# Kernel tuning notes

Hardware: AMD Instinct MI355X
Metric: run time of the kernel (lower is better)

## Reference

```python
import jax, jax.numpy as jnp
import numpy as np


def setup_inputs() -> dict:
    key = jax.random.key(0)
    kf, kz = jax.random.split(key)
    B, H, S = 32, 1024, 2048
    f = jax.random.uniform(kf, (B, H, S), dtype=jnp.float32)  # forget gate in [0,1]
    z = jax.random.normal(kz, (B, H, S), dtype=jnp.float32)
    return {"f": f, "z": z}


def reference(f, z):
    # Original: permute (B,H,S)->(S,B,H), run h_t = (1-f_t)*z_t + f_t*h_{t-1}
    # with h_{-1}=0, then permute back (S,B,H)->(B,H,S).
    fs = jnp.moveaxis(f, 2, 0)  # (S,B,H)
    zs = jnp.moveaxis(z, 2, 0)  # (S,B,H)
    h0 = jnp.zeros(f.shape[:2], dtype=f.dtype)  # (B,H)

    def step(h_prev, fz):
        ft, zt = fz
        h = (1.0 - ft) * zt + ft * h_prev
        return h, h

    _, hs = jax.lax.scan(step, h0, (fs, zs))  # hs: (S,B,H)
    return jnp.moveaxis(hs, 0, 2)  # (B,H,S)
```

## Files before the change

kernel.cpp:

```cpp
#include <hip/hip_runtime.h>


#define SEQ_LEN 2048
#define THREADS 256
#define PER_THREAD 8

__global__ __launch_bounds__(THREADS) void fpool_scan_kernel(
    const float* __restrict__ f,
    const float* __restrict__ z,
    float* __restrict__ out)
{
    const long long row  = blockIdx.x;
    const long long base = row * (long long)SEQ_LEN;
    const int tid  = threadIdx.x;
    const int lane = tid & 63;
    const int wave = tid >> 6;

    const float4* f4 = reinterpret_cast<const float4*>(f + base);
    const float4* z4 = reinterpret_cast<const float4*>(z + base);
    float4 fa = f4[tid * 2 + 0];
    float4 fb = f4[tid * 2 + 1];
    float4 za = z4[tid * 2 + 0];
    float4 zb = z4[tid * 2 + 1];

    float av[PER_THREAD] = {fa.x, fa.y, fa.z, fa.w, fb.x, fb.y, fb.z, fb.w};
    float zv[PER_THREAD] = {za.x, za.y, za.z, za.w, zb.x, zb.y, zb.z, zb.w};

    float P[PER_THREAD], L[PER_THREAD];
    float p = 1.0f, l = 0.0f;
#pragma unroll
    for (int i = 0; i < PER_THREAD; ++i) {
        const float ai = av[i];
        const float bi = (1.0f - ai) * zv[i];
        l = fmaf(ai, l, bi);
        p = p * ai;
        P[i] = p;
        L[i] = l;
    }

    float cp = p, cl = l;
#pragma unroll
    for (int d = 1; d < 64; d <<= 1) {
        float pp = __shfl_up(cp, d);
        float pl = __shfl_up(cl, d);
        if (lane >= d) {
            cl = fmaf(cp, pl, cl);
            cp = cp * pp;
        }
    }

    __shared__ float wp[THREADS / 64];
    __shared__ float wl[THREADS / 64];
    if (lane == 63) { wp[wave] = cp; wl[wave] = cl; }
    __syncthreads();

    float h_wave = 0.0f;
#pragma unroll
    for (int w = 0; w < THREADS / 64; ++w) {
        if (w < wave) h_wave = fmaf(wp[w], h_wave, wl[w]);
    }

    float ep = __shfl_up(cp, 1);
    float el = __shfl_up(cl, 1);
    if (lane == 0) { ep = 1.0f; el = 0.0f; }

    const float h_in = fmaf(ep, h_wave, el);

    float o[PER_THREAD];
#pragma unroll
    for (int i = 0; i < PER_THREAD; ++i) o[i] = fmaf(P[i], h_in, L[i]);

    float4* o4 = reinterpret_cast<float4*>(out + base);
    o4[tid * 2 + 0] = make_float4(o[0], o[1], o[2], o[3]);
    o4[tid * 2 + 1] = make_float4(o[4], o[5], o[6], o[7]);
}

extern "C" void kernel_launch(void* const* d_in, const int* in_sizes, int n_in,
                              void* d_out, int out_size, void* d_ws, size_t ws_size,
                              hipStream_t stream) {
    const float* f = reinterpret_cast<const float*>(d_in[0]);
    const float* z = reinterpret_cast<const float*>(d_in[1]);
    float* out = reinterpret_cast<float*>(d_out);

    const long long total = in_sizes[0];
    const int rows = (int)(total / SEQ_LEN);

    fpool_scan_kernel<<<rows, THREADS, 0, stream>>>(f, z, out);
}
```

Baseline: 142.5 us.

## Split each row into two coalesced halves with separate block scans and nontemporal stores

Each thread now loads one float4 from each half of the row, so every load instruction is fully contiguous across the block instead of strided by two float4s per thread. Each half gets its own wave-shuffle and cross-wave scan, and the second half is seeded with the total of the first. Outputs go out through nontemporal stores to avoid polluting cache. In exchange the shuffle scan work and block barriers are doubled, which adds latency to a kernel that is mostly bound by memory bandwidth.

```diff
diff --git a/kernel.cpp b/kernel.cpp
--- a/kernel.cpp
+++ b/kernel.cpp
@@ -3,7 +3,44 @@
 
 #define SEQ_LEN 2048
 #define THREADS 256
-#define PER_THREAD 8
+#define CHUNK   4
+
+typedef float fvec4 __attribute__((ext_vector_type(4)));
+
+__device__ __forceinline__ void scan_block(
+    float p, float l, int lane, int wave,
+    float* wp, float* wl,
+    float& ep, float& el, float& tp, float& tl)
+{
+    float cp = p, cl = l;
+#pragma unroll
+    for (int d = 1; d < 64; d <<= 1) {
+        float pp = __shfl_up(cp, d);
+        float pl = __shfl_up(cl, d);
+        if (lane >= d) {
+            cl = fmaf(cp, pl, cl);
+            cp = cp * pp;
+        }
+    }
+    if (lane == 63) { wp[wave] = cp; wl[wave] = cl; }
+    __syncthreads();
+
+    ep = __shfl_up(cp, 1);
+    el = __shfl_up(cl, 1);
+    if (lane == 0) { ep = 1.0f; el = 0.0f; }
+
+    float bp = 1.0f, bl = 0.0f;
+    float qp = 1.0f, ql = 0.0f;
+#pragma unroll
+    for (int w = 0; w < THREADS / 64; ++w) {
+        float wpw = wp[w], wlw = wl[w];
+        if (w < wave) { bl = fmaf(wpw, bl, wlw); bp *= wpw; }
+        ql = fmaf(wpw, ql, wlw); qp *= wpw;
+    }
+    el = fmaf(ep, bl, el);
+    ep = ep * bp;
+    tp = qp; tl = ql;
+}
 
 __global__ __launch_bounds__(THREADS) void fpool_scan_kernel(
     const float* __restrict__ f,
@@ -18,61 +55,64 @@
 
     const float4* f4 = reinterpret_cast<const float4*>(f + base);
     const float4* z4 = reinterpret_cast<const float4*>(z + base);
-    float4 fa = f4[tid * 2 + 0];
-    float4 fb = f4[tid * 2 + 1];
-    float4 za = z4[tid * 2 + 0];
-    float4 zb = z4[tid * 2 + 1];
+    fvec4* o4 = reinterpret_cast<fvec4*>(out + base);
 
-    float av[PER_THREAD] = {fa.x, fa.y, fa.z, fa.w, fb.x, fb.y, fb.z, fb.w};
-    float zv[PER_THREAD] = {za.x, za.y, za.z, za.w, zb.x, zb.y, zb.z, zb.w};
+    float4 fA = f4[tid];
+    float4 zA = z4[tid];
+    float4 fB = f4[THREADS + tid];
+    float4 zB = z4[THREADS + tid];
 
-    float P[PER_THREAD], L[PER_THREAD];
-    float p = 1.0f, l = 0.0f;
+    float aA[CHUNK] = {fA.x, fA.y, fA.z, fA.w};
+    float vA[CHUNK] = {zA.x, zA.y, zA.z, zA.w};
+    float aB[CHUNK] = {fB.x, fB.y, fB.z, fB.w};
+    float vB[CHUNK] = {zB.x, zB.y, zB.z, zB.w};
+
+    float PA[CHUNK], LA[CHUNK], PB[CHUNK], LB[CHUNK];
+    {
+        float p = 1.0f, l = 0.0f;
 #pragma unroll
-    for (int i = 0; i < PER_THREAD; ++i) {
-        const float ai = av[i];
-        const float bi = (1.0f - ai) * zv[i];
-        l = fmaf(ai, l, bi);
-        p = p * ai;
-        P[i] = p;
-        L[i] = l;
+        for (int i = 0; i < CHUNK; ++i) {
+            l = fmaf(aA[i], l, (1.0f - aA[i]) * vA[i]);
+            p = p * aA[i];
+            PA[i] = p; LA[i] = l;
+        }
     }
-
-    float cp = p, cl = l;
+    {
+        float p = 1.0f, l = 0.0f;
 #pragma unroll
-    for (int d = 1; d < 64; d <<= 1) {
-        float pp = __shfl_up(cp, d);
-        float pl = __shfl_up(cl, d);
-        if (lane >= d) {
-            cl = fmaf(cp, pl, cl);
-            cp = cp * pp;
+        for (int i = 0; i < CHUNK; ++i) {
+            l = fmaf(aB[i], l, (1.0f - aB[i]) * vB[i]);
+            p = p * aB[i];
+            PB[i] = p; LB[i] = l;
         }
     }
 
-    __shared__ float wp[THREADS / 64];
-    __shared__ float wl[THREADS / 64];
-    if (lane == 63) { wp[wave] = cp; wl[wave] = cl; }
-    __syncthreads();
+    __shared__ float wpA[THREADS / 64], wlA[THREADS / 64];
+    __shared__ float wpB[THREADS / 64], wlB[THREADS / 64];
 
-    float h_wave = 0.0f;
-#pragma unroll
-    for (int w = 0; w < THREADS / 64; ++w) {
-        if (w < wave) h_wave = fmaf(wp[w], h_wave, wl[w]);
-    }
+    float epA, elA, tpA, tlA;
+    scan_block(PA[CHUNK - 1], LA[CHUNK - 1], lane, wave, wpA, wlA,
+               epA, elA, tpA, tlA);
+    const float hA = elA;
 
-    float ep = __shfl_up(cp, 1);
-    float el = __shfl_up(cl, 1);
-    if (lane == 0) { ep = 1.0f; el = 0.0f; }
+    float epB, elB, tpB, tlB;
+    scan_block(PB[CHUNK - 1], LB[CHUNK - 1], lane, wave, wpB, wlB,
+               epB, elB, tpB, tlB);
+    const float h_half = tlA;
+    const float hB = fmaf(epB, h_half, elB);
 
-    const float h_in = fmaf(ep, h_wave, el);
+    fvec4 oA, oB;
+    oA.x = fmaf(PA[0], hA, LA[0]);
+    oA.y = fmaf(PA[1], hA, LA[1]);
+    oA.z = fmaf(PA[2], hA, LA[2]);
+    oA.w = fmaf(PA[3], hA, LA[3]);
+    oB.x = fmaf(PB[0], hB, LB[0]);
+    oB.y = fmaf(PB[1], hB, LB[1]);
+    oB.z = fmaf(PB[2], hB, LB[2]);
+    oB.w = fmaf(PB[3], hB, LB[3]);
 
-    float o[PER_THREAD];
-#pragma unroll
-    for (int i = 0; i < PER_THREAD; ++i) o[i] = fmaf(P[i], h_in, L[i]);
-
-    float4* o4 = reinterpret_cast<float4*>(out + base);
-    o4[tid * 2 + 0] = make_float4(o[0], o[1], o[2], o[3]);
-    o4[tid * 2 + 1] = make_float4(o[4], o[5], o[6], o[7]);
+    __builtin_nontemporal_store(oA, &o4[tid]);
+    __builtin_nontemporal_store(oB, &o4[THREADS + tid]);
 }
 
 extern "C" void kernel_launch(void* const* d_in, const int* in_sizes, int n_in,
```

New measurement: 143.5 us. No clear change (+0.7%).
